# Kernel optimization log

Hardware: AMD Instinct MI355X
Metric: run time of the kernel (lower is better)

Reference implementation:

```python
import jax, jax.numpy as jnp
import numpy as np

OUT = 7            # output_size per dim
RATIO = 2          # sampling_ratio
CANON_S = 160.0    # canonical_scale
CANON_L = 4.0      # canonical_level
EPS = 1e-6
K_MIN, K_MAX = 2, 5                      # from scales 1/4 .. 1/32
SCALES = (0.25, 0.125, 0.0625, 0.03125)  # inferred vs 256^3 image


def _coords(start, bsz):
    # start,bsz: [N] -> sample coords [N, OUT*RATIO]
    offs = (jnp.arange(OUT)[:, None] + (jnp.arange(RATIO) + 0.5) / RATIO).reshape(-1)
    return start[:, None] + offs[None, :] * bsz[:, None]


def _axis(c, dim):
    # torchvision border handling: zero outside [-1, dim], clamp inside
    valid = ((c > -1.0) & (c < dim)).astype(c.dtype)
    cc = jnp.clip(c, 0.0, dim - 1.0)
    lo = jnp.floor(cc).astype(jnp.int32)
    hi = jnp.minimum(lo + 1, int(dim) - 1)
    frac = cc - lo
    return lo, hi, (1.0 - frac) * valid, frac * valid


def roi_align_3d(feat, batch_idx, boxes, scale):
    # feat [B,C,X,Y,Z]; boxes [N,6] = (x1,y1,z1,x2,y2,z2) in image coords
    N = boxes.shape[0]
    C = feat.shape[1]
    dims = feat.shape[2:]
    start = boxes[:, :3] * scale
    size = jnp.maximum(boxes[:, 3:] * scale - start, 1.0)
    bsz = size / OUT  # [N,3] bin sizes
    f = jnp.transpose(feat, (0, 2, 3, 4, 1))  # [B,X,Y,Z,C]
    ax = [_axis(_coords(start[:, d], bsz[:, d]), float(dims[d])) for d in range(3)]
    b = batch_idx
    acc = jnp.zeros((N, OUT * RATIO, OUT * RATIO, OUT * RATIO, C), feat.dtype)
    for ix, wx in ((ax[0][0], ax[0][2]), (ax[0][1], ax[0][3])):
        for iy, wy in ((ax[1][0], ax[1][2]), (ax[1][1], ax[1][3])):
            for iz, wz in ((ax[2][0], ax[2][2]), (ax[2][1], ax[2][3])):
                v = f[b[:, None, None, None], ix[:, :, None, None],
                      iy[:, None, :, None], iz[:, None, None, :]]  # [N,Sx,Sy,Sz,C]
                w = wx[:, :, None, None] * wy[:, None, :, None] * wz[:, None, None, :]
                acc = acc + w[..., None] * v
    # average sampling points within each bin
    acc = acc.reshape(N, OUT, RATIO, OUT, RATIO, OUT, RATIO, C).mean(axis=(2, 4, 6))
    return jnp.transpose(acc, (0, 4, 1, 2, 3))  # [N,C,OUT,OUT,OUT]


def level_map(boxes):
    vol = ((boxes[:, 3] - boxes[:, 0]) * (boxes[:, 4] - boxes[:, 1])
           * (boxes[:, 5] - boxes[:, 2]))
    s = jnp.cbrt(vol)
    lvl = jnp.floor(CANON_L + jnp.log2(s / CANON_S) + EPS)
    return jnp.clip(lvl, K_MIN, K_MAX).astype(jnp.int32) - K_MIN


def setup_inputs() -> dict:
    key = jax.random.key(0)
    ks = jax.random.split(key, 6)
    N, C = 256, 64
    feat0 = jax.random.normal(ks[0], (1, C, 64, 64, 64), jnp.float32)
    feat1 = jax.random.normal(ks[1], (1, C, 32, 32, 32), jnp.float32)
    feat2 = jax.random.normal(ks[2], (1, C, 16, 16, 16), jnp.float32)
    feat3 = jax.random.normal(ks[3], (1, C, 8, 8, 8), jnp.float32)
    sz = 10.0 + jax.random.uniform(ks[4], (N, 3)) * 240.0   # edge lengths
    p1 = jax.random.uniform(ks[5], (N, 3)) * (256.0 - sz)
    boxes = jnp.concatenate([p1, p1 + sz], axis=1)  # valid (x1<x2 etc.) in 256^3 image
    return {"feat0": feat0, "feat1": feat1, "feat2": feat2, "feat3": feat3, "boxes": boxes}


def reference(feat0, feat1, feat2, feat3, boxes):
    feats = (feat0, feat1, feat2, feat3)
    levels = level_map(boxes)
    b = jnp.zeros(boxes.shape[0], dtype=jnp.int32)  # single image -> all batch id 0
    out = jnp.zeros((boxes.shape[0], feat0.shape[1], OUT, OUT, OUT), feat0.dtype)
    for l, (feat, sc) in enumerate(zip(feats, SCALES)):
        pooled = roi_align_3d(feat, b, boxes, sc)
        mask = (levels == l).astype(pooled.dtype)[:, None, None, None, None]
        out = out + mask * pooled
    return out
```

## Files before the change

kernel.cpp:

```cpp
#include <hip/hip_runtime.h>
#include <math.h>

#define OUT 7
#define NVOX 343
#define NCHUNK 22

typedef unsigned short u16;
typedef unsigned int u32;

__device__ __forceinline__ u16 f32_to_bf16(float f) {
    u32 u = __float_as_uint(f);
    u32 r = (u + 0x7fffu + ((u >> 16) & 1u)) >> 16;
    return (u16)r;
}
__device__ __forceinline__ float bf16_to_f32(u16 h) {
    return __uint_as_float(((u32)h) << 16);
}

__device__ __forceinline__ void axis_samp(float c, float fdim, int dim,
                                          int& lo, float& w0, float& w1) {
    float valid = (c > -1.0f && c < fdim) ? 1.0f : 0.0f;
    float cc = fminf(fmaxf(c, 0.0f), fdim - 1.0f);
    lo = (int)floorf(cc);
    float fr = cc - (float)lo;
    w0 = (1.0f - fr) * valid;
    w1 = fr * valid;
}

__device__ __forceinline__ void box_setup(const float* bp,
                                          int d0, int d1, int d2_, int d3,
                                          int& l, int& dim, float& fdim,
                                          float& st0, float& st1, float& st2,
                                          float& bs0, float& bs1, float& bs2) {
    float b0 = bp[0], b1 = bp[1], b2 = bp[2];
    float b3 = bp[3], b4 = bp[4], b5 = bp[5];
    float vol = (b3 - b0) * (b4 - b1) * (b5 - b2);
    float s = cbrtf(vol);
    float lvl = floorf(4.0f + log2f(s / 160.0f) + 1e-6f);
    lvl = fminf(fmaxf(lvl, 2.0f), 5.0f);
    l = (int)lvl - 2;
    float scale;
    if (l == 0)      { dim = d0;  scale = 0.25f;    }
    else if (l == 1) { dim = d1;  scale = 0.125f;   }
    else if (l == 2) { dim = d2_; scale = 0.0625f;  }
    else             { dim = d3;  scale = 0.03125f; }
    fdim = (float)dim;
    st0 = b0 * scale; st1 = b1 * scale; st2 = b2 * scale;
    float e0 = fmaxf(b3 * scale - st0, 1.0f);
    float e1 = fmaxf(b4 * scale - st1, 1.0f);
    float e2 = fmaxf(b5 * scale - st2, 1.0f);
    bs0 = e0 * (1.0f / OUT); bs1 = e1 * (1.0f / OUT); bs2 = e2 * (1.0f / OUT);
}

#define LDSF 11776
#define FBLK 512

__global__ __launch_bounds__(FBLK) void roi_align_fallback_kernel(
    const float* __restrict__ f0, const float* __restrict__ f1,
    const float* __restrict__ f2, const float* __restrict__ f3,
    const float* __restrict__ boxes, float* __restrict__ out,
    int N, int C, int d0, int d1, int d2_, int d3)
{
    __shared__ float lds[LDSF];
    const int c   = blockIdx.x;
    const int n   = blockIdx.y;
    const int tid = threadIdx.x;

    int l, dim; float fdim, st0, st1, st2, bs0, bs1, bs2;
    box_setup(boxes + n * 6, d0, d1, d2_, d3,
              l, dim, fdim, st0, st1, st2, bs0, bs1, bs2);
    const float* f = (l == 0) ? f0 : (l == 1) ? f1 : (l == 2) ? f2 : f3;

    const int dsq = dim * dim;
    const size_t dcube = (size_t)dim * dsq;
    const float* fc = f + (size_t)c * dcube;

    int x0 = (int)floorf(fminf(fmaxf(st0 + 0.25f * bs0, 0.0f), fdim - 1.0f));
    int x1 = min((int)floorf(fminf(fmaxf(st0 + 6.75f * bs0, 0.0f), fdim - 1.0f)) + 1, dim - 1);
    int y0 = (int)floorf(fminf(fmaxf(st1 + 0.25f * bs1, 0.0f), fdim - 1.0f));
    int y1 = min((int)floorf(fminf(fmaxf(st1 + 6.75f * bs1, 0.0f), fdim - 1.0f)) + 1, dim - 1);
    int z0 = (int)floorf(fminf(fmaxf(st2 + 0.25f * bs2, 0.0f), fdim - 1.0f));
    int z1 = min((int)floorf(fminf(fmaxf(st2 + 6.75f * bs2, 0.0f), fdim - 1.0f)) + 1, dim - 1);

    int nx = x1 - x0 + 1, ny = y1 - y0 + 1, nz = z1 - z0 + 1;
    int nzp = nz + 1;
    int nynzp = ny * nzp;
    int nrows = nx * ny;
    int nregp = nrows * nzp;

    int xl[2], yl[2], zl[2];
    float xw0[2], xw1[2], yw0[2], yw1[2], zw0[2], zw1[2];
    if (tid < NVOX) {
        int oz = tid % OUT;
        int oy = (tid / OUT) % OUT;
        int ox = tid / (OUT * OUT);
        #pragma unroll
        for (int r = 0; r < 2; ++r) {
            float off = 0.25f + 0.5f * (float)r;
            axis_samp(st0 + ((float)ox + off) * bs0, fdim, dim, xl[r], xw0[r], xw1[r]);
            axis_samp(st1 + ((float)oy + off) * bs1, fdim, dim, yl[r], yw0[r], yw1[r]);
            axis_samp(st2 + ((float)oz + off) * bs2, fdim, dim, zl[r], zw0[r], zw1[r]);
        }
    }

    if (nregp <= LDSF) {
        float rnzp = 1.0f / (float)nzp;
        float rny  = 1.0f / (float)ny;
        for (int e = tid; e < nregp; e += FBLK) {
            int row = (int)((float)e * rnzp);
            int zz = e - row * nzp;
            if (zz < 0)        { row -= 1; zz += nzp; }
            else if (zz >= nzp){ row += 1; zz -= nzp; }
            int rx = (int)((float)row * rny);
            int ry = row - rx * ny;
            if (ry < 0)        { rx -= 1; ry += ny; }
            else if (ry >= ny) { rx += 1; ry -= ny; }
            int zsrc = min(zz, nz - 1);
            lds[e] = fc[((size_t)(x0 + rx) * dim + (y0 + ry)) * dim + (z0 + zsrc)];
        }
        __syncthreads();

        if (tid < NVOX) {
            int XL[2], XH[2], YL[2], YH[2], ZL[2];
            #pragma unroll
            for (int r = 0; r < 2; ++r) {
                XL[r] = (xl[r] - x0) * nynzp;
                XH[r] = (min(xl[r] + 1, dim - 1) - x0) * nynzp;
                YL[r] = (yl[r] - y0) * nzp;
                YH[r] = (min(yl[r] + 1, dim - 1) - y0) * nzp;
                ZL[r] = zl[r] - z0;
            }
            float acc = 0.0f;
            #pragma unroll
            for (int rx2 = 0; rx2 < 2; ++rx2) {
                #pragma unroll
                for (int ry2 = 0; ry2 < 2; ++ry2) {
                    #pragma unroll
                    for (int rz2 = 0; rz2 < 2; ++rz2) {
                        const float* pll = lds + (XL[rx2] + YL[ry2] + ZL[rz2]);
                        const float* plh = lds + (XL[rx2] + YH[ry2] + ZL[rz2]);
                        const float* phl = lds + (XH[rx2] + YL[ry2] + ZL[rz2]);
                        const float* phh = lds + (XH[rx2] + YH[ry2] + ZL[rz2]);
                        float wz0 = zw0[rz2], wz1 = zw1[rz2];
                        float vx0 = yw0[ry2] * (wz0 * pll[0] + wz1 * pll[1])
                                  + yw1[ry2] * (wz0 * plh[0] + wz1 * plh[1]);
                        float vx1 = yw0[ry2] * (wz0 * phl[0] + wz1 * phl[1])
                                  + yw1[ry2] * (wz0 * phh[0] + wz1 * phh[1]);
                        acc += xw0[rx2] * vx0 + xw1[rx2] * vx1;
                    }
                }
            }
            out[((size_t)n * C + c) * NVOX + tid] = acc * 0.125f;
        }
    } else {
        if (tid < NVOX) {
            float acc = 0.0f;
            #pragma unroll
            for (int rx2 = 0; rx2 < 2; ++rx2) {
                const float* pxl = fc + (size_t)xl[rx2] * dsq;
                const float* pxh = fc + (size_t)min(xl[rx2] + 1, dim - 1) * dsq;
                float wx0 = xw0[rx2], wx1 = xw1[rx2];
                #pragma unroll
                for (int ry2 = 0; ry2 < 2; ++ry2) {
                    int ryl = yl[ry2] * dim;
                    int ryh = min(yl[ry2] + 1, dim - 1) * dim;
                    float wy0 = yw0[ry2], wy1 = yw1[ry2];
                    #pragma unroll
                    for (int rz2 = 0; rz2 < 2; ++rz2) {
                        int bZL = zl[rz2], bZH = min(zl[rz2] + 1, dim - 1);
                        float wz0 = zw0[rz2], wz1 = zw1[rz2];
                        float vx0 = wy0 * (wz0 * pxl[ryl + bZL] + wz1 * pxl[ryl + bZH])
                                  + wy1 * (wz0 * pxl[ryh + bZL] + wz1 * pxl[ryh + bZH]);
                        float vx1 = wy0 * (wz0 * pxh[ryl + bZL] + wz1 * pxh[ryl + bZH])
                                  + wy1 * (wz0 * pxh[ryh + bZL] + wz1 * pxh[ryh + bZH]);
                        acc += wx0 * vx0 + wx1 * vx1;
                    }
                }
            }
            out[((size_t)n * C + c) * NVOX + tid] = acc * 0.125f;
        }
    }
}

__global__ __launch_bounds__(256) void transpose_bf16_kernel(
    const float* __restrict__ f0, const float* __restrict__ f1,
    const float* __restrict__ f2, const float* __restrict__ f3,
    u16* __restrict__ ws,
    int t1, int t2, int t3,
    long S0, long S1, long S2, long S3,
    long off0, long off1, long off2, long off3)
{
    __shared__ u16 tile[64 * 65];
    int b = blockIdx.x;
    const float* src; u16* dst; long S; int tloc;
    if (b < t1)      { src = f0; dst = ws + off0; S = S0; tloc = b; }
    else if (b < t2) { src = f1; dst = ws + off1; S = S1; tloc = b - t1; }
    else if (b < t3) { src = f2; dst = ws + off2; S = S2; tloc = b - t2; }
    else             { src = f3; dst = ws + off3; S = S3; tloc = b - t3; }

    long s0 = (long)tloc * 64;
    int lane  = threadIdx.x & 63;
    int chunk = threadIdx.x >> 6;
    #pragma unroll
    for (int k = 0; k < 16; ++k) {
        int ch = chunk * 16 + k;
        tile[lane * 65 + ch] = f32_to_bf16(src[(size_t)ch * S + s0 + lane]);
    }
    __syncthreads();
    #pragma unroll
    for (int k = 0; k < 16; ++k) {
        int s = chunk * 16 + k;
        dst[(s0 + s) * 64 + lane] = tile[s * 65 + lane];
    }
}


#define LSTRIDE 66

struct Grp { float w0, w1, w2, w3; ushort4 v0, v1, v2, v3; };

__device__ __forceinline__ Grp issue_grp(const int2* L, int g,
                                         const char* base, int qoff) {
    int4 a = *(const int4*)(L + (g << 2));
    int4 b = *(const int4*)(L + (g << 2) + 2);
    Grp r;
    r.w0 = __int_as_float(a.y); r.v0 = *(const ushort4*)(base + (a.x + qoff));
    r.w1 = __int_as_float(a.w); r.v1 = *(const ushort4*)(base + (a.z + qoff));
    r.w2 = __int_as_float(b.y); r.v2 = *(const ushort4*)(base + (b.x + qoff));
    r.w3 = __int_as_float(b.w); r.v3 = *(const ushort4*)(base + (b.z + qoff));
    return r;
}

__device__ __forceinline__ void consume_grp(const Grp& g, float4& acc) {
    acc.x = fmaf(g.w0, bf16_to_f32(g.v0.x), acc.x);
    acc.y = fmaf(g.w0, bf16_to_f32(g.v0.y), acc.y);
    acc.z = fmaf(g.w0, bf16_to_f32(g.v0.z), acc.z);
    acc.w = fmaf(g.w0, bf16_to_f32(g.v0.w), acc.w);
    acc.x = fmaf(g.w1, bf16_to_f32(g.v1.x), acc.x);
    acc.y = fmaf(g.w1, bf16_to_f32(g.v1.y), acc.y);
    acc.z = fmaf(g.w1, bf16_to_f32(g.v1.z), acc.z);
    acc.w = fmaf(g.w1, bf16_to_f32(g.v1.w), acc.w);
    acc.x = fmaf(g.w2, bf16_to_f32(g.v2.x), acc.x);
    acc.y = fmaf(g.w2, bf16_to_f32(g.v2.y), acc.y);
    acc.z = fmaf(g.w2, bf16_to_f32(g.v2.z), acc.z);
    acc.w = fmaf(g.w2, bf16_to_f32(g.v2.w), acc.w);
    acc.x = fmaf(g.w3, bf16_to_f32(g.v3.x), acc.x);
    acc.y = fmaf(g.w3, bf16_to_f32(g.v3.y), acc.y);
    acc.z = fmaf(g.w3, bf16_to_f32(g.v3.z), acc.z);
    acc.w = fmaf(g.w3, bf16_to_f32(g.v3.w), acc.w);
}

__global__ __launch_bounds__(256, 4) void roi_align_cl_kernel(
    const u16* __restrict__ ws, const float* __restrict__ boxes,
    float* __restrict__ out, int N, int C,
    int d0, int d1, int d2_, int d3,
    long off0, long off1, long off2, long off3)
{
    __shared__ int2  lst[16 * LSTRIDE];
    __shared__ float axw[16][3][4];
    __shared__ int   axo[16][3][4];
    __shared__ int   hdrN[16];
    __shared__ int   hdrM[16];
    __shared__ float hdrR[16][2];
    __shared__ float ldsout[64 * 17];

    const int n    = blockIdx.x;
    const int cb   = blockIdx.y * 16;
    const int tid  = threadIdx.x;
    const int quad = tid & 15;
    const int slot = tid >> 4;

    int l, dim; float fdim, st0, st1, st2, bs0, bs1, bs2;
    box_setup(boxes + n * 6, d0, d1, d2_, d3,
              l, dim, fdim, st0, st1, st2, bs0, bs1, bs2);
    const long loff = (l == 0) ? off0 : (l == 1) ? off1 : (l == 2) ? off2 : off3;
    const int dsq = dim * dim;

    if (tid < 16) {
        const int s = tid;
        int v = min(cb + s, NVOX - 1);
        int o2 = v % OUT;
        int t7 = v / OUT;
        int o1 = t7 % OUT;
        int o0 = t7 / OUT;
        const int   strB[3] = { dsq * 128, dim * 128, 128 };
        const float oA[3]   = { (float)o0, (float)o1, (float)o2 };
        const float sA[3]   = { st0, st1, st2 };
        const float bA[3]   = { bs0, bs1, bs2 };
        int m3[3];
        #pragma unroll
        for (int a = 0; a < 3; ++a) {
            int lo0, lo1; float w00, w01, w10, w11;
            axis_samp(sA[a] + (oA[a] + 0.25f) * bA[a], fdim, dim, lo0, w00, w01);
            axis_samp(sA[a] + (oA[a] + 0.75f) * bA[a], fdim, dim, lo1, w10, w11);
            int hi0 = min(lo0 + 1, dim - 1);
            int hi1 = min(lo1 + 1, dim - 1);
            int sa, sb; float qa, qb;
            if (hi0 <= lo1) { sa = hi0; qa = w01; sb = lo1; qb = w10; }
            else            { sa = lo1; qa = w10; sb = hi0; qb = w01; }
            int m = 0;
            int cur = lo0; float wacc = w00;
            if (sa == cur) wacc += qa;
            else {
                if (wacc > 0.0f) { axw[s][a][m] = wacc; axo[s][a][m] = cur * strB[a]; ++m; }
                cur = sa; wacc = qa;
            }
            if (sb == cur) wacc += qb;
            else {
                if (wacc > 0.0f) { axw[s][a][m] = wacc; axo[s][a][m] = cur * strB[a]; ++m; }
                cur = sb; wacc = qb;
            }
            if (hi1 == cur) wacc += w11;
            else {
                if (wacc > 0.0f) { axw[s][a][m] = wacc; axo[s][a][m] = cur * strB[a]; ++m; }
                cur = hi1; wacc = w11;
            }
            if (wacc > 0.0f) { axw[s][a][m] = wacc; axo[s][a][m] = cur * strB[a]; ++m; }
            m3[a] = m;
        }
        int nT = m3[0] * m3[1] * m3[2];
        hdrN[s] = (nT + 7) & ~7;
        hdrM[s] = m3[0] | (m3[1] << 8) | (m3[2] << 16);
        hdrR[s][0] = __builtin_amdgcn_rcpf((float)max(m3[1] * m3[2], 1));
        hdrR[s][1] = __builtin_amdgcn_rcpf((float)max(m3[2], 1));
    }
    __syncthreads();

    if (cb + slot < NVOX) {
        const int pm  = hdrM[slot];
        const int my  = (pm >> 8) & 255, mz = (pm >> 16) & 255, mx = pm & 255;
        const int myz = my * mz;
        const int nT  = mx * myz;
        const int nT8 = hdrN[slot];
        const float rYZ = hdrR[slot][0], rZ = hdrR[slot][1];
        for (int t = quad; t < nT8; t += 16) {
            int off = 0; float w = 0.0f;
            if (t < nT) {
                int i   = (int)(((float)t + 0.5f) * rYZ);
                int rem = t - i * myz;
                int j   = (int)(((float)rem + 0.5f) * rZ);
                int k   = rem - j * mz;
                w   = axw[slot][0][i] * axw[slot][1][j] * axw[slot][2][k];
                off = axo[slot][0][i] + axo[slot][1][j] + axo[slot][2][k];
            }
            lst[slot * LSTRIDE + t] = make_int2(off, __float_as_int(w));
        }
    }
    __syncthreads();

    const bool active = (cb + slot) < NVOX;
    if (active) {
        const char* base = (const char*)(ws + loff);
        const int qoff   = quad * 8;
        const int2* L    = lst + slot * LSTRIDE;
        const int nT8    = hdrN[slot];
        float4 acc = { 0.f, 0.f, 0.f, 0.f };
        if (nT8 > 0) {
            const int nG = nT8 >> 2;
            Grp A = issue_grp(L, 0, base, qoff);
            int g = 1;
            for (; g + 1 < nG; g += 2) {
                Grp B = issue_grp(L, g, base, qoff);
                consume_grp(A, acc);
                A = issue_grp(L, g + 1, base, qoff);
                consume_grp(B, acc);
            }
            {
                Grp B = issue_grp(L, g, base, qoff);
                consume_grp(A, acc);
                consume_grp(B, acc);
            }
        }
        int chb = quad * 4;
        ldsout[(chb + 0) * 17 + slot] = acc.x * 0.125f;
        ldsout[(chb + 1) * 17 + slot] = acc.y * 0.125f;
        ldsout[(chb + 2) * 17 + slot] = acc.z * 0.125f;
        ldsout[(chb + 3) * 17 + slot] = acc.w * 0.125f;
    }
    __syncthreads();

    int nv = min(16, NVOX - cb);
    #pragma unroll
    for (int k = 0; k < 4; ++k) {
        int flat = k * 256 + tid;
        int ch = flat >> 4, vs = flat & 15;
        if (vs < nv)
            out[((size_t)n * C + ch) * NVOX + cb + vs] = ldsout[ch * 17 + vs];
    }
}

extern "C" void kernel_launch(void* const* d_in, const int* in_sizes, int n_in,
                              void* d_out, int out_size, void* d_ws, size_t ws_size,
                              hipStream_t stream) {
    const float* f0 = (const float*)d_in[0];
    const float* f1 = (const float*)d_in[1];
    const float* f2 = (const float*)d_in[2];
    const float* f3 = (const float*)d_in[3];
    const float* boxes = (const float*)d_in[4];
    float* out = (float*)d_out;

    int N = in_sizes[4] / 6;
    int C = out_size / (N * NVOX);

    auto cdim = [&](int sz) {
        int per_c = sz / C;
        return (int)(cbrtf((float)per_c) + 0.5f);
    };
    int d0 = cdim(in_sizes[0]);
    int d1 = cdim(in_sizes[1]);
    int d2 = cdim(in_sizes[2]);
    int d3 = cdim(in_sizes[3]);

    long S0 = (long)d0 * d0 * d0, S1 = (long)d1 * d1 * d1;
    long S2 = (long)d2 * d2 * d2, S3 = (long)d3 * d3 * d3;
    long off0 = 0, off1 = S0 * C, off2 = off1 + S1 * C, off3 = off2 + S2 * C;
    size_t need = (size_t)(off3 + S3 * C) * sizeof(u16);

    bool fast = (C == 64) && (ws_size >= need) &&
                (S0 % 64 == 0) && (S1 % 64 == 0) && (S2 % 64 == 0) && (S3 % 64 == 0);

    if (fast) {
        u16* ws = (u16*)d_ws;
        int t1 = (int)(S0 / 64);
        int t2 = t1 + (int)(S1 / 64);
        int t3 = t2 + (int)(S2 / 64);
        int tt = t3 + (int)(S3 / 64);
        transpose_bf16_kernel<<<tt, 256, 0, stream>>>(f0, f1, f2, f3, ws,
                                                      t1, t2, t3,
                                                      S0, S1, S2, S3,
                                                      off0, off1, off2, off3);
        dim3 grid(N, NCHUNK);
        roi_align_cl_kernel<<<grid, 256, 0, stream>>>(ws, boxes, out, N, C,
                                                      d0, d1, d2, d3,
                                                      off0, off1, off2, off3);
    } else {
        dim3 grid(C, N);
        roi_align_fallback_kernel<<<grid, FBLK, 0, stream>>>(f0, f1, f2, f3, boxes, out,
                                                             N, C, d0, d1, d2, d3);
    }
}
```

Measured before the change: 145.9 us.

## Parallelize axis setup across 48 threads and triple-buffer gathers with wave-uniform trip counts

Axis sample/weight setup is spread over 48 threads, one per (voxel, axis), instead of 16 threads each looping over three axes. The 1/8 averaging factor is folded into the x-axis weights so the per-channel scale at the end goes away. Tap counts are padded to multiples of 4 instead of 8, and each group of four slots uses the maximum count among them, so loop bounds are uniform across a wavefront. The gather loop moves from double to triple buffering to keep more loads in flight, at the cost of more registers and some wasted zero-weight taps.

```diff
diff --git a/kernel.cpp b/kernel.cpp
--- a/kernel.cpp
+++ b/kernel.cpp
@@ -259,6 +259,7 @@
     __shared__ int2  lst[16 * LSTRIDE];
     __shared__ float axw[16][3][4];
     __shared__ int   axo[16][3][4];
+    __shared__ int   axm[16][3];
     __shared__ int   hdrN[16];
     __shared__ int   hdrM[16];
     __shared__ float hdrR[16][2];
@@ -276,64 +277,69 @@
     const long loff = (l == 0) ? off0 : (l == 1) ? off1 : (l == 2) ? off2 : off3;
     const int dsq = dim * dim;
 
-    if (tid < 16) {
-        const int s = tid;
+    if (tid < 48) {
+        const int s = tid & 15;
+        const int a = tid >> 4;
         int v = min(cb + s, NVOX - 1);
         int o2 = v % OUT;
         int t7 = v / OUT;
         int o1 = t7 % OUT;
         int o0 = t7 / OUT;
-        const int   strB[3] = { dsq * 128, dim * 128, 128 };
-        const float oA[3]   = { (float)o0, (float)o1, (float)o2 };
-        const float sA[3]   = { st0, st1, st2 };
-        const float bA[3]   = { bs0, bs1, bs2 };
-        int m3[3];
-        #pragma unroll
-        for (int a = 0; a < 3; ++a) {
-            int lo0, lo1; float w00, w01, w10, w11;
-            axis_samp(sA[a] + (oA[a] + 0.25f) * bA[a], fdim, dim, lo0, w00, w01);
-            axis_samp(sA[a] + (oA[a] + 0.75f) * bA[a], fdim, dim, lo1, w10, w11);
-            int hi0 = min(lo0 + 1, dim - 1);
-            int hi1 = min(lo1 + 1, dim - 1);
-            int sa, sb; float qa, qb;
-            if (hi0 <= lo1) { sa = hi0; qa = w01; sb = lo1; qb = w10; }
-            else            { sa = lo1; qa = w10; sb = hi0; qb = w01; }
-            int m = 0;
-            int cur = lo0; float wacc = w00;
-            if (sa == cur) wacc += qa;
-            else {
-                if (wacc > 0.0f) { axw[s][a][m] = wacc; axo[s][a][m] = cur * strB[a]; ++m; }
-                cur = sa; wacc = qa;
-            }
-            if (sb == cur) wacc += qb;
-            else {
-                if (wacc > 0.0f) { axw[s][a][m] = wacc; axo[s][a][m] = cur * strB[a]; ++m; }
-                cur = sb; wacc = qb;
-            }
-            if (hi1 == cur) wacc += w11;
-            else {
-                if (wacc > 0.0f) { axw[s][a][m] = wacc; axo[s][a][m] = cur * strB[a]; ++m; }
-                cur = hi1; wacc = w11;
-            }
-            if (wacc > 0.0f) { axw[s][a][m] = wacc; axo[s][a][m] = cur * strB[a]; ++m; }
-            m3[a] = m;
-        }
-        int nT = m3[0] * m3[1] * m3[2];
-        hdrN[s] = (nT + 7) & ~7;
-        hdrM[s] = m3[0] | (m3[1] << 8) | (m3[2] << 16);
-        hdrR[s][0] = __builtin_amdgcn_rcpf((float)max(m3[1] * m3[2], 1));
-        hdrR[s][1] = __builtin_amdgcn_rcpf((float)max(m3[2], 1));
+        const int   strB = (a == 0) ? dsq * 128 : (a == 1) ? dim * 128 : 128;
+        const float oA   = (a == 0) ? (float)o0 : (a == 1) ? (float)o1 : (float)o2;
+        const float sA   = (a == 0) ? st0 : (a == 1) ? st1 : st2;
+        const float bA   = (a == 0) ? bs0 : (a == 1) ? bs1 : bs2;
+        const float sc   = (a == 0) ? 0.125f : 1.0f;
+
+        int lo0, lo1; float w00, w01, w10, w11;
+        axis_samp(sA + (oA + 0.25f) * bA, fdim, dim, lo0, w00, w01);
+        axis_samp(sA + (oA + 0.75f) * bA, fdim, dim, lo1, w10, w11);
+        int hi0 = min(lo0 + 1, dim - 1);
+        int hi1 = min(lo1 + 1, dim - 1);
+        int sa, sb; float qa, qb;
+        if (hi0 <= lo1) { sa = hi0; qa = w01; sb = lo1; qb = w10; }
+        else            { sa = lo1; qa = w10; sb = hi0; qb = w01; }
+        int m = 0;
+        int cur = lo0; float wacc = w00;
+        if (sa == cur) wacc += qa;
+        else {
+            if (wacc > 0.0f) { axw[s][a][m] = wacc * sc; axo[s][a][m] = cur * strB; ++m; }
+            cur = sa; wacc = qa;
+        }
+        if (sb == cur) wacc += qb;
+        else {
+            if (wacc > 0.0f) { axw[s][a][m] = wacc * sc; axo[s][a][m] = cur * strB; ++m; }
+            cur = sb; wacc = qb;
+        }
+        if (hi1 == cur) wacc += w11;
+        else {
+            if (wacc > 0.0f) { axw[s][a][m] = wacc * sc; axo[s][a][m] = cur * strB; ++m; }
+            cur = hi1; wacc = w11;
+        }
+        if (wacc > 0.0f) { axw[s][a][m] = wacc * sc; axo[s][a][m] = cur * strB; ++m; }
+        axm[s][a] = m;
+    }
+    if (tid < 16) {
+        int mx = axm[tid][0], my = axm[tid][1], mz = axm[tid][2];
+        int nT = mx * my * mz;
+        hdrN[tid] = (nT + 3) & ~3;
+        hdrM[tid] = mx | (my << 8) | (mz << 16);
+        hdrR[tid][0] = __builtin_amdgcn_rcpf((float)max(my * mz, 1));
+        hdrR[tid][1] = __builtin_amdgcn_rcpf((float)max(mz, 1));
     }
     __syncthreads();
 
-    if (cb + slot < NVOX) {
+    const int ws4  = slot & ~3;
+    const int NT8w = max(max(hdrN[ws4], hdrN[ws4 + 1]),
+                         max(hdrN[ws4 + 2], hdrN[ws4 + 3]));
+
+    {
         const int pm  = hdrM[slot];
         const int my  = (pm >> 8) & 255, mz = (pm >> 16) & 255, mx = pm & 255;
         const int myz = my * mz;
         const int nT  = mx * myz;
-        const int nT8 = hdrN[slot];
         const float rYZ = hdrR[slot][0], rZ = hdrR[slot][1];
-        for (int t = quad; t < nT8; t += 16) {
+        for (int t = quad; t < NT8w; t += 16) {
             int off = 0; float w = 0.0f;
             if (t < nT) {
                 int i   = (int)(((float)t + 0.5f) * rYZ);
@@ -348,34 +354,48 @@
     }
     __syncthreads();
 
-    const bool active = (cb + slot) < NVOX;
-    if (active) {
+    {
         const char* base = (const char*)(ws + loff);
         const int qoff   = quad * 8;
         const int2* L    = lst + slot * LSTRIDE;
-        const int nT8    = hdrN[slot];
+        const int NG     = NT8w >> 2;
         float4 acc = { 0.f, 0.f, 0.f, 0.f };
-        if (nT8 > 0) {
-            const int nG = nT8 >> 2;
+        if (NG >= 3) {
             Grp A = issue_grp(L, 0, base, qoff);
-            int g = 1;
-            for (; g + 1 < nG; g += 2) {
-                Grp B = issue_grp(L, g, base, qoff);
-                consume_grp(A, acc);
-                A = issue_grp(L, g + 1, base, qoff);
-                consume_grp(B, acc);
-            }
-            {
-                Grp B = issue_grp(L, g, base, qoff);
-                consume_grp(A, acc);
-                consume_grp(B, acc);
-            }
+            Grp B = issue_grp(L, 1, base, qoff);
+            Grp C = issue_grp(L, 2, base, qoff);
+            int g = 3;
+            for (; g + 2 < NG; g += 3) {
+                Grp D = issue_grp(L, g,     base, qoff); consume_grp(A, acc); A = D;
+                Grp E = issue_grp(L, g + 1, base, qoff); consume_grp(B, acc); B = E;
+                Grp F = issue_grp(L, g + 2, base, qoff); consume_grp(C, acc); C = F;
+            }
+            int r = NG - g;
+            if (r == 2) {
+                Grp D = issue_grp(L, g, base, qoff);
+                Grp E = issue_grp(L, g + 1, base, qoff);
+                consume_grp(A, acc); consume_grp(B, acc); consume_grp(C, acc);
+                consume_grp(D, acc); consume_grp(E, acc);
+            } else if (r == 1) {
+                Grp D = issue_grp(L, g, base, qoff);
+                consume_grp(A, acc); consume_grp(B, acc); consume_grp(C, acc);
+                consume_grp(D, acc);
+            } else {
+                consume_grp(A, acc); consume_grp(B, acc); consume_grp(C, acc);
+            }
+        } else if (NG == 2) {
+            Grp A = issue_grp(L, 0, base, qoff);
+            Grp B = issue_grp(L, 1, base, qoff);
+            consume_grp(A, acc); consume_grp(B, acc);
+        } else if (NG == 1) {
+            Grp A = issue_grp(L, 0, base, qoff);
+            consume_grp(A, acc);
         }
         int chb = quad * 4;
-        ldsout[(chb + 0) * 17 + slot] = acc.x * 0.125f;
-        ldsout[(chb + 1) * 17 + slot] = acc.y * 0.125f;
-        ldsout[(chb + 2) * 17 + slot] = acc.z * 0.125f;
-        ldsout[(chb + 3) * 17 + slot] = acc.w * 0.125f;
+        ldsout[(chb + 0) * 17 + slot] = acc.x;
+        ldsout[(chb + 1) * 17 + slot] = acc.y;
+        ldsout[(chb + 2) * 17 + slot] = acc.z;
+        ldsout[(chb + 3) * 17 + slot] = acc.w;
     }
     __syncthreads();
 
```

Result: slower. 151.5 us (+3.9%).

## Use 512-thread blocks over 32 voxels with parallel axis setup and wave-local lists

Applied to the files above, without the earlier changes.

Each block now covers 32 output voxels with 512 threads, halving the number of chunks per box. The per-axis sample merging is spread over 96 threads, one per voxel-axis pair, instead of 16 threads each looping over three axes. Each wave takes the maximum tap count across its slots with shuffles, so its gather list can be built and consumed without a block-wide barrier. The 1/8 averaging factor is folded into the x-axis weights. Padded slots past the last voxel now do redundant gathers on a clamped voxel, and wave-uniform tap counts add some padding work.

```diff
diff --git a/kernel.cpp b/kernel.cpp
--- a/kernel.cpp
+++ b/kernel.cpp
@@ -3,7 +3,8 @@
 
 #define OUT 7
 #define NVOX 343
-#define NCHUNK 22
+#define VB 32
+#define NCH2 11
 
 typedef unsigned short u16;
 typedef unsigned int u32;
@@ -250,142 +251,137 @@
     acc.w = fmaf(g.w3, bf16_to_f32(g.v3.w), acc.w);
 }
 
-__global__ __launch_bounds__(256, 4) void roi_align_cl_kernel(
+__global__ __launch_bounds__(512, 4) void roi_align_cl_kernel(
     const u16* __restrict__ ws, const float* __restrict__ boxes,
     float* __restrict__ out, int N, int C,
     int d0, int d1, int d2_, int d3,
     long off0, long off1, long off2, long off3)
 {
-    __shared__ int2  lst[16 * LSTRIDE];
-    __shared__ float axw[16][3][4];
-    __shared__ int   axo[16][3][4];
-    __shared__ int   hdrN[16];
-    __shared__ int   hdrM[16];
-    __shared__ float hdrR[16][2];
-    __shared__ float ldsout[64 * 17];
+    __shared__ __align__(16) int2 lst[VB * LSTRIDE];
+    __shared__ int2  awo[VB][3][4];
+    __shared__ int   axm[VB][3];
+    __shared__ int   bxl[1];
+    __shared__ float ldsout[64 * (VB + 1)];
 
     const int n    = blockIdx.x;
-    const int cb   = blockIdx.y * 16;
+    const int cb   = blockIdx.y * VB;
     const int tid  = threadIdx.x;
     const int quad = tid & 15;
     const int slot = tid >> 4;
 
-    int l, dim; float fdim, st0, st1, st2, bs0, bs1, bs2;
-    box_setup(boxes + n * 6, d0, d1, d2_, d3,
-              l, dim, fdim, st0, st1, st2, bs0, bs1, bs2);
-    const long loff = (l == 0) ? off0 : (l == 1) ? off1 : (l == 2) ? off2 : off3;
-    const int dsq = dim * dim;
-
-    if (tid < 16) {
-        const int s = tid;
+    if (tid < 96) {
+        int l, dim; float fdim, st0, st1, st2, bs0, bs1, bs2;
+        box_setup(boxes + n * 6, d0, d1, d2_, d3,
+                  l, dim, fdim, st0, st1, st2, bs0, bs1, bs2);
+        if (tid == 0) bxl[0] = l;
+        const int dsq = dim * dim;
+
+        const int s = tid & 31;
+        const int a = tid >> 5;
         int v = min(cb + s, NVOX - 1);
         int o2 = v % OUT;
         int t7 = v / OUT;
         int o1 = t7 % OUT;
         int o0 = t7 / OUT;
-        const int   strB[3] = { dsq * 128, dim * 128, 128 };
-        const float oA[3]   = { (float)o0, (float)o1, (float)o2 };
-        const float sA[3]   = { st0, st1, st2 };
-        const float bA[3]   = { bs0, bs1, bs2 };
-        int m3[3];
-        #pragma unroll
-        for (int a = 0; a < 3; ++a) {
-            int lo0, lo1; float w00, w01, w10, w11;
-            axis_samp(sA[a] + (oA[a] + 0.25f) * bA[a], fdim, dim, lo0, w00, w01);
-            axis_samp(sA[a] + (oA[a] + 0.75f) * bA[a], fdim, dim, lo1, w10, w11);
-            int hi0 = min(lo0 + 1, dim - 1);
-            int hi1 = min(lo1 + 1, dim - 1);
-            int sa, sb; float qa, qb;
-            if (hi0 <= lo1) { sa = hi0; qa = w01; sb = lo1; qb = w10; }
-            else            { sa = lo1; qa = w10; sb = hi0; qb = w01; }
-            int m = 0;
-            int cur = lo0; float wacc = w00;
-            if (sa == cur) wacc += qa;
-            else {
-                if (wacc > 0.0f) { axw[s][a][m] = wacc; axo[s][a][m] = cur * strB[a]; ++m; }
-                cur = sa; wacc = qa;
-            }
-            if (sb == cur) wacc += qb;
-            else {
-                if (wacc > 0.0f) { axw[s][a][m] = wacc; axo[s][a][m] = cur * strB[a]; ++m; }
-                cur = sb; wacc = qb;
-            }
-            if (hi1 == cur) wacc += w11;
-            else {
-                if (wacc > 0.0f) { axw[s][a][m] = wacc; axo[s][a][m] = cur * strB[a]; ++m; }
-                cur = hi1; wacc = w11;
-            }
-            if (wacc > 0.0f) { axw[s][a][m] = wacc; axo[s][a][m] = cur * strB[a]; ++m; }
-            m3[a] = m;
-        }
-        int nT = m3[0] * m3[1] * m3[2];
-        hdrN[s] = (nT + 7) & ~7;
-        hdrM[s] = m3[0] | (m3[1] << 8) | (m3[2] << 16);
-        hdrR[s][0] = __builtin_amdgcn_rcpf((float)max(m3[1] * m3[2], 1));
-        hdrR[s][1] = __builtin_amdgcn_rcpf((float)max(m3[2], 1));
+        const int   strB = (a == 0) ? dsq * 128 : (a == 1) ? dim * 128 : 128;
+        const float oA   = (a == 0) ? (float)o0 : (a == 1) ? (float)o1 : (float)o2;
+        const float sA   = (a == 0) ? st0 : (a == 1) ? st1 : st2;
+        const float bA   = (a == 0) ? bs0 : (a == 1) ? bs1 : bs2;
+        const float sc   = (a == 0) ? 0.125f : 1.0f;
+
+        int lo0, lo1; float w00, w01, w10, w11;
+        axis_samp(sA + (oA + 0.25f) * bA, fdim, dim, lo0, w00, w01);
+        axis_samp(sA + (oA + 0.75f) * bA, fdim, dim, lo1, w10, w11);
+        int hi0 = min(lo0 + 1, dim - 1);
+        int hi1 = min(lo1 + 1, dim - 1);
+        int sa, sb; float qa, qb;
+        if (hi0 <= lo1) { sa = hi0; qa = w01; sb = lo1; qb = w10; }
+        else            { sa = lo1; qa = w10; sb = hi0; qb = w01; }
+        int m = 0;
+        int cur = lo0; float wacc = w00;
+        if (sa == cur) wacc += qa;
+        else {
+            if (wacc > 0.0f) { awo[s][a][m] = make_int2(cur * strB, __float_as_int(wacc * sc)); ++m; }
+            cur = sa; wacc = qa;
+        }
+        if (sb == cur) wacc += qb;
+        else {
+            if (wacc > 0.0f) { awo[s][a][m] = make_int2(cur * strB, __float_as_int(wacc * sc)); ++m; }
+            cur = sb; wacc = qb;
+        }
+        if (hi1 == cur) wacc += w11;
+        else {
+            if (wacc > 0.0f) { awo[s][a][m] = make_int2(cur * strB, __float_as_int(wacc * sc)); ++m; }
+            cur = hi1; wacc = w11;
+        }
+        if (wacc > 0.0f) { awo[s][a][m] = make_int2(cur * strB, __float_as_int(wacc * sc)); ++m; }
+        axm[s][a] = m;
     }
     __syncthreads();
 
-    if (cb + slot < NVOX) {
-        const int pm  = hdrM[slot];
-        const int my  = (pm >> 8) & 255, mz = (pm >> 16) & 255, mx = pm & 255;
+    const int l = bxl[0];
+    const long loff = (l == 0) ? off0 : (l == 1) ? off1 : (l == 2) ? off2 : off3;
+    int NTw;
+    {
+        const int mx = axm[slot][0], my = axm[slot][1], mz = axm[slot][2];
         const int myz = my * mz;
         const int nT  = mx * myz;
-        const int nT8 = hdrN[slot];
-        const float rYZ = hdrR[slot][0], rZ = hdrR[slot][1];
-        for (int t = quad; t < nT8; t += 16) {
+        int nT8 = (nT + 7) & ~7;
+        int m1  = max(nT8, __shfl_xor(nT8, 16));
+        NTw     = max(m1, __shfl_xor(m1, 32));
+        const float rYZ = __builtin_amdgcn_rcpf((float)max(myz, 1));
+        const float rZ  = __builtin_amdgcn_rcpf((float)max(mz, 1));
+        for (int t = quad; t < NTw; t += 16) {
             int off = 0; float w = 0.0f;
             if (t < nT) {
                 int i   = (int)(((float)t + 0.5f) * rYZ);
                 int rem = t - i * myz;
                 int j   = (int)(((float)rem + 0.5f) * rZ);
                 int k   = rem - j * mz;
-                w   = axw[slot][0][i] * axw[slot][1][j] * axw[slot][2][k];
-                off = axo[slot][0][i] + axo[slot][1][j] + axo[slot][2][k];
+                int2 ei = awo[slot][0][i];
+                int2 ej = awo[slot][1][j];
+                int2 ek = awo[slot][2][k];
+                w   = __int_as_float(ei.y) * __int_as_float(ej.y) * __int_as_float(ek.y);
+                off = ei.x + ej.x + ek.x;
             }
             lst[slot * LSTRIDE + t] = make_int2(off, __float_as_int(w));
         }
     }
-    __syncthreads();
-
-    const bool active = (cb + slot) < NVOX;
-    if (active) {
+
+    {
         const char* base = (const char*)(ws + loff);
         const int qoff   = quad * 8;
         const int2* L    = lst + slot * LSTRIDE;
-        const int nT8    = hdrN[slot];
+        const int NG     = NTw >> 2;
         float4 acc = { 0.f, 0.f, 0.f, 0.f };
-        if (nT8 > 0) {
-            const int nG = nT8 >> 2;
+        if (NG >= 2) {
             Grp A = issue_grp(L, 0, base, qoff);
             int g = 1;
-            for (; g + 1 < nG; g += 2) {
+            for (; g + 1 < NG; g += 2) {
                 Grp B = issue_grp(L, g, base, qoff);
                 consume_grp(A, acc);
                 A = issue_grp(L, g + 1, base, qoff);
                 consume_grp(B, acc);
             }
-            {
-                Grp B = issue_grp(L, g, base, qoff);
-                consume_grp(A, acc);
-                consume_grp(B, acc);
-            }
+            Grp B = issue_grp(L, g, base, qoff);
+            consume_grp(A, acc);
+            consume_grp(B, acc);
         }
         int chb = quad * 4;
-        ldsout[(chb + 0) * 17 + slot] = acc.x * 0.125f;
-        ldsout[(chb + 1) * 17 + slot] = acc.y * 0.125f;
-        ldsout[(chb + 2) * 17 + slot] = acc.z * 0.125f;
-        ldsout[(chb + 3) * 17 + slot] = acc.w * 0.125f;
+        ldsout[(chb + 0) * (VB + 1) + slot] = acc.x;
+        ldsout[(chb + 1) * (VB + 1) + slot] = acc.y;
+        ldsout[(chb + 2) * (VB + 1) + slot] = acc.z;
+        ldsout[(chb + 3) * (VB + 1) + slot] = acc.w;
     }
     __syncthreads();
 
-    int nv = min(16, NVOX - cb);
+    const int nv = min(VB, NVOX - cb);
     #pragma unroll
     for (int k = 0; k < 4; ++k) {
-        int flat = k * 256 + tid;
-        int ch = flat >> 4, vs = flat & 15;
+        int flat = k * 512 + tid;
+        int ch = flat >> 5, vs = flat & 31;
         if (vs < nv)
-            out[((size_t)n * C + ch) * NVOX + cb + vs] = ldsout[ch * 17 + vs];
+            out[((size_t)n * C + ch) * NVOX + cb + vs] = ldsout[ch * (VB + 1) + vs];
     }
 }
 
@@ -429,8 +425,8 @@
                                                       t1, t2, t3,
                                                       S0, S1, S2, S3,
                                                       off0, off1, off2, off3);
-        dim3 grid(N, NCHUNK);
-        roi_align_cl_kernel<<<grid, 256, 0, stream>>>(ws, boxes, out, N, C,
+        dim3 grid(N, NCH2);
+        roi_align_cl_kernel<<<grid, 512, 0, stream>>>(ws, boxes, out, N, C,
                                                       d0, d1, d2, d3,
                                                       off0, off1, off2, off3);
     } else {
```

After: 146.8 us. No clear change (+0.6%).
